# Kernel optimization log

Hardware: AMD Instinct MI355X
Metric: run time of the kernel (lower is better)

Reference implementation:

```python
import jax, jax.numpy as jnp
import numpy as np
from jax import lax


def setup_inputs() -> dict:
    key = jax.random.key(0)
    ks = jax.random.split(key, 13)
    B, L, H, E, V, T = 32, 256, 512, 512, 32000, 64
    s = 0.05
    return {
        "z": jax.random.normal(ks[0], (B, L), jnp.float32),
        "embedding": jax.random.normal(ks[1], (V, E), jnp.float32) * s,
        "Wh": jax.random.normal(ks[2], (H, L), jnp.float32) * s,
        "bh": jax.random.normal(ks[3], (H,), jnp.float32) * s,
        "Wc": jax.random.normal(ks[4], (H, L), jnp.float32) * s,
        "bc": jax.random.normal(ks[5], (H,), jnp.float32) * s,
        "Wih": jax.random.normal(ks[6], (4 * H, E), jnp.float32) * s,
        "Whh": jax.random.normal(ks[7], (4 * H, H), jnp.float32) * s,
        "bih": jax.random.normal(ks[8], (4 * H,), jnp.float32) * s,
        "bhh": jax.random.normal(ks[9], (4 * H,), jnp.float32) * s,
        "Wfc": jax.random.normal(ks[10], (V, H), jnp.float32) * s,
        "bfc": jax.random.normal(ks[11], (V,), jnp.float32) * s,
        "context_length": T,
    }


def reference(z, embedding, Wh, bh, Wc, bc, Wih, Whh, bih, bhh, Wfc, bfc, context_length):
    # project latent to initial LSTM state: [B, H]
    h0 = z @ Wh.T + bh
    c0 = z @ Wc.T + bc
    b_gates = bih + bhh

    def step(carry, _):
        h, c, x = carry  # each [B, H] / [B, E]
        gates = x @ Wih.T + h @ Whh.T + b_gates  # [B, 4H] (pytorch gate order i,f,g,o)
        i, f, g, o = jnp.split(gates, 4, axis=-1)
        c_new = jax.nn.sigmoid(f) * c + jax.nn.sigmoid(i) * jnp.tanh(g)
        h_new = jax.nn.sigmoid(o) * jnp.tanh(c_new)
        logits = h_new @ Wfc.T + bfc  # [B, V]
        pred = jnp.argmax(logits, axis=-1)  # greedy token
        x_new = embedding[pred]  # [B, E]
        return (h_new, c_new, x_new), logits

    # first step feeds h itself as the input (x is None in torch code)
    _, logits = lax.scan(step, (h0, c0, h0), None, length=context_length)
    return jnp.transpose(logits, (1, 0, 2))  # [B, T, V]
```

## Files before the change

### kernel.cpp

```cpp
#include <hip/hip_runtime.h>
#include <hip/hip_bf16.h>
#include <cstdint>
#include <cstddef>

#define NB 32
#define NL 256
#define NH 512
#define NE 512
#define NV 32000
#define NT 64
#define NJ 2048
#define NK 1024
#define NKT 16

typedef __attribute__((ext_vector_type(8))) short bf16x8;
typedef __attribute__((ext_vector_type(4))) float f32x4;


__device__ __forceinline__ unsigned int sortable_f32(float f) {
  unsigned int s = __float_as_uint(f);
  return (s & 0x80000000u) ? ~s : (s | 0x80000000u);
}

__device__ __forceinline__ unsigned long long pack_key(float f, int v) {
  return ((unsigned long long)sortable_f32(f) << 32) |
         (unsigned long long)(unsigned int)(~v);
}

__device__ __forceinline__ unsigned long long shfl_xor_u64(unsigned long long x, int m) {
  unsigned int lo = (unsigned int)x;
  unsigned int hi = (unsigned int)(x >> 32);
  lo = __shfl_xor(lo, m, 64);
  hi = __shfl_xor(hi, m, 64);
  return ((unsigned long long)hi << 32) | lo;
}

__device__ __forceinline__ uint32_t pack_hi16(uint32_t u0, uint32_t u1) {
  return __builtin_amdgcn_perm(u1, u0, 0x07060302u);
}

__device__ __forceinline__ void split3(float4 wa, float4 wb,
                                       bf16x8& A1, bf16x8& A2, bf16x8& A3) {
  union U { uint32_t w[4]; bf16x8 v; };
  U u1, u2, u3;
  float e[8] = {wa.x, wa.y, wa.z, wa.w, wb.x, wb.y, wb.z, wb.w};
#pragma unroll
  for (int p = 0; p < 4; ++p) {
    float e0 = e[2 * p], e1 = e[2 * p + 1];
    uint32_t a0 = __float_as_uint(e0), a1 = __float_as_uint(e1);
    u1.w[p] = pack_hi16(a0, a1);
    float r0 = e0 - __uint_as_float(a0 & 0xffff0000u);
    float r1 = e1 - __uint_as_float(a1 & 0xffff0000u);
    uint32_t b0 = __float_as_uint(r0), b1 = __float_as_uint(r1);
    u2.w[p] = pack_hi16(b0, b1);
    float q0 = r0 - __uint_as_float(b0 & 0xffff0000u);
    float q1 = r1 - __uint_as_float(b1 & 0xffff0000u);
    u3.w[p] = pack_hi16(__float_as_uint(q0), __float_as_uint(q1));
  }
  A1 = u1.v; A2 = u2.v; A3 = u3.v;
}

__device__ __forceinline__ unsigned long long load_key(const unsigned long long* p) {
  return __hip_atomic_load(p, __ATOMIC_ACQUIRE, __HIP_MEMORY_SCOPE_AGENT);
}


__global__ void k_init(const float* __restrict__ z, const float* __restrict__ Wh,
                       const float* __restrict__ bh, const float* __restrict__ Wc,
                       const float* __restrict__ bc, float* __restrict__ hbuf,
                       float* __restrict__ cbuf, unsigned long long* __restrict__ keys) {
  int idx = blockIdx.x * 256 + threadIdx.x;
  int b = idx >> 9, hh = idx & 511;
  const float* zr  = z + b * NL;
  const float* whr = Wh + hh * NL;
  const float* wcr = Wc + hh * NL;
  float ah = 0.f, ac = 0.f;
  for (int k = 0; k < NL; ++k) {
    float zv = zr[k];
    ah += zv * whr[k];
    ac += zv * wcr[k];
  }
  hbuf[b * NH + hh] = ah + bh[hh];
  cbuf[b * NH + hh] = ac + bc[hh];
  if (idx < 64)
    __hip_atomic_store(&keys[idx], 0ULL, __ATOMIC_RELEASE, __HIP_MEMORY_SCOPE_AGENT);
}

__global__ void k_transposeW(const float* __restrict__ Wih, const float* __restrict__ Whh,
                             float* __restrict__ WT) {
  __shared__ float tile[32][33];
  int j0 = blockIdx.x * 32;
  int k0 = blockIdx.y * 32;
  int tx = threadIdx.x & 31;
  int ty = threadIdx.x >> 5;
  for (int r = ty; r < 32; r += 8) {
    int j = j0 + r, k = k0 + tx;
    tile[r][tx] = (k < NE) ? Wih[j * NE + k] : Whh[j * NH + (k - NE)];
  }
  __syncthreads();
  for (int r = ty; r < 32; r += 8) {
    int k = k0 + r, j = j0 + tx;
    WT[(size_t)k * NJ + j] = tile[tx][r];
  }
}

__global__ void k_packW32(const float* __restrict__ Wfc, float* __restrict__ Wp32) {
  int bid = blockIdx.x;
  int tid = threadIdx.x;
  int lane = tid & 63, wv = tid >> 6;
  int r16 = lane & 15, g = lane >> 4;
  const float* wr = Wfc + (size_t)(bid * 16 + r16) * NH + g * 8;
#pragma unroll
  for (int q = 0; q < 4; ++q) {
    int kq = wv * 4 + q;
    float4 wa = *(const float4*)(wr + kq * 32);
    float4 wb = *(const float4*)(wr + kq * 32 + 4);
    float* dst = Wp32 + ((size_t)(bid * 16 + kq) << 9) + lane * 8;
    *(float4*)dst = wa;
    *(float4*)(dst + 4) = wb;
  }
}

__global__ void k_gates(const float* __restrict__ WT, const float* __restrict__ emb,
                        const float* __restrict__ hbuf, const unsigned long long* __restrict__ keys,
                        float* __restrict__ partials, int step) {
  __shared__ unsigned int spred[NB];
  int tid  = threadIdx.x;
  int jthr = tid & 31, bthr = tid >> 5;
  int j0 = blockIdx.x * 128 + jthr * 4;
  int k0 = blockIdx.y * 64;
  int b0 = bthr * 4;
  const float* hin = hbuf + (size_t)(step & 1) * NB * NH;
  const bool isx = (k0 < NE);

  if (step > 0 && isx && tid < NB) {
    unsigned long long key = load_key(&keys[((step - 1) & 1) * NB + tid]);
    unsigned int pred = ~(unsigned int)(key & 0xFFFFFFFFu);
    if (pred >= NV) pred = 0;
    spred[tid] = pred;
  }
  __syncthreads();

  const float* xp[4];
#pragma unroll
  for (int i = 0; i < 4; ++i) {
    int b = b0 + i;
    if (!isx) {
      xp[i] = hin + (size_t)b * NH - NE;
    } else if (step == 0) {
      xp[i] = hin + (size_t)b * NE;
    } else {
      xp[i] = emb + (size_t)spred[b] * NE;
    }
  }

  float acc[4][4];
#pragma unroll
  for (int jj = 0; jj < 4; ++jj)
#pragma unroll
    for (int i = 0; i < 4; ++i) acc[jj][i] = 0.f;

#pragma unroll 4
  for (int k = k0; k < k0 + 64; ++k) {
    float4 w = *(const float4*)(WT + (size_t)k * NJ + j0);
#pragma unroll
    for (int i = 0; i < 4; ++i) {
      float xv = xp[i][k];
      acc[0][i] += w.x * xv;
      acc[1][i] += w.y * xv;
      acc[2][i] += w.z * xv;
      acc[3][i] += w.w * xv;
    }
  }

  int kt = blockIdx.y;
#pragma unroll
  for (int jj = 0; jj < 4; ++jj)
#pragma unroll
    for (int i = 0; i < 4; ++i)
      partials[((size_t)(j0 + jj) * NB + (b0 + i)) * NKT + kt] = acc[jj][i];
}

__global__ void k_cell(const float* __restrict__ partials, const float* __restrict__ bih,
                       const float* __restrict__ bhh, float* __restrict__ hbuf,
                       float* __restrict__ cbuf, unsigned short* __restrict__ hs,
                       unsigned long long* __restrict__ keys, int step) {
  int idx = blockIdx.x * 256 + threadIdx.x;
  int b = idx >> 9, hh = idx & 511;
  float g4[4];
#pragma unroll
  for (int g = 0; g < 4; ++g) {
    int j = g * NH + hh;
    const float4* p4 = (const float4*)(partials + ((size_t)j * NB + b) * NKT);
    float4 a0 = p4[0], a1 = p4[1], a2 = p4[2], a3 = p4[3];
    float s = ((a0.x + a0.y) + (a0.z + a0.w)) + ((a1.x + a1.y) + (a1.z + a1.w)) +
              ((a2.x + a2.y) + (a2.z + a2.w)) + ((a3.x + a3.y) + (a3.z + a3.w));
    g4[g] = s + bih[j] + bhh[j];
  }
  float ig = 1.0f / (1.0f + expf(-g4[0]));
  float fg = 1.0f / (1.0f + expf(-g4[1]));
  float gg = tanhf(g4[2]);
  float og = 1.0f / (1.0f + expf(-g4[3]));
  float c  = cbuf[b * NH + hh];
  float cn = fg * c + ig * gg;
  float hn = og * tanhf(cn);
  cbuf[b * NH + hh] = cn;
  hbuf[(size_t)((step + 1) & 1) * NB * NH + b * NH + hh] = hn;

  uint32_t u = __float_as_uint(hn);
  float r1 = hn - __uint_as_float(u & 0xffff0000u);
  uint32_t u2 = __float_as_uint(r1);
  float r2 = r1 - __uint_as_float(u2 & 0xffff0000u);
  uint32_t u3 = __float_as_uint(r2);
  hs[0 * NB * NH + b * NH + hh] = (unsigned short)(u >> 16);
  hs[1 * NB * NH + b * NH + hh] = (unsigned short)(u2 >> 16);
  hs[2 * NB * NH + b * NH + hh] = (unsigned short)(u3 >> 16);

  if (idx < NB)
    __hip_atomic_store(&keys[(step & 1) * NB + idx], 0ULL,
                       __ATOMIC_RELEASE, __HIP_MEMORY_SCOPE_AGENT);
}

__global__ __launch_bounds__(512, 1) void k_logits3(
    const float* __restrict__ Wp32, const float* __restrict__ bfc,
    const unsigned short* __restrict__ hs, float* __restrict__ out,
    unsigned long long* __restrict__ keys, int step) {
  __shared__ __align__(16) unsigned short H[3][32][520];
  __shared__ __align__(16) float tbuf[32][132];
  __shared__ unsigned long long kmax[32];

  const int tid = threadIdx.x, bid = blockIdx.x;
  const int lane = tid & 63, wid = tid >> 6;
  const int r16 = lane & 15, g = lane >> 4;

  const int wg = bid * 8 + wid;
  const float* wbase = Wp32 + ((size_t)wg << 13) + lane * 8;

  float4 wa0 = *(const float4*)(wbase);
  float4 wb0 = *(const float4*)(wbase + 4);
  float4 wan = *(const float4*)(wbase + 512);
  float4 wbn = *(const float4*)(wbase + 512 + 4);

#pragma unroll
  for (int i = 0; i < 12; ++i) {
    int idx = tid + i * 512;
    int s = idx >> 11, rem = idx & 2047;
    int row = rem >> 6, ch = rem & 63;
    float4 d = *(const float4*)(hs + (size_t)s * (NB * NH) + row * NH + ch * 8);
    *(float4*)(&H[s][row][ch * 8]) = d;
  }
  if (tid < 32) kmax[tid] = 0ULL;

  bf16x8 Acur[3];
  split3(wa0, wb0, Acur[0], Acur[1], Acur[2]);
  __syncthreads();

  f32x4 acc0 = {0.f, 0.f, 0.f, 0.f};
  f32x4 acc1 = {0.f, 0.f, 0.f, 0.f};

#pragma unroll
  for (int kq = 0; kq < 16; ++kq) {
    float4 wa2, wb2;
    if (kq < 14) {
      wa2 = *(const float4*)(wbase + (size_t)(kq + 2) * 512);
      wb2 = *(const float4*)(wbase + (size_t)(kq + 2) * 512 + 4);
    }
    bf16x8 Anx[3];
    if (kq < 15) split3(wan, wbn, Anx[0], Anx[1], Anx[2]);

    const int ko = kq * 32 + g * 8;
    bf16x8 B1n0 = *(const bf16x8*)(&H[0][r16][ko]);
    bf16x8 B1n1 = *(const bf16x8*)(&H[0][r16 + 16][ko]);
    bf16x8 B2n0 = *(const bf16x8*)(&H[1][r16][ko]);
    bf16x8 B2n1 = *(const bf16x8*)(&H[1][r16 + 16][ko]);
    bf16x8 B3n0 = *(const bf16x8*)(&H[2][r16][ko]);
    bf16x8 B3n1 = *(const bf16x8*)(&H[2][r16 + 16][ko]);

    acc0 = __builtin_amdgcn_mfma_f32_16x16x32_bf16(Acur[0], B1n0, acc0, 0, 0, 0);
    acc0 = __builtin_amdgcn_mfma_f32_16x16x32_bf16(Acur[0], B2n0, acc0, 0, 0, 0);
    acc0 = __builtin_amdgcn_mfma_f32_16x16x32_bf16(Acur[1], B1n0, acc0, 0, 0, 0);
    acc0 = __builtin_amdgcn_mfma_f32_16x16x32_bf16(Acur[1], B2n0, acc0, 0, 0, 0);
    acc0 = __builtin_amdgcn_mfma_f32_16x16x32_bf16(Acur[0], B3n0, acc0, 0, 0, 0);
    acc0 = __builtin_amdgcn_mfma_f32_16x16x32_bf16(Acur[2], B1n0, acc0, 0, 0, 0);

    acc1 = __builtin_amdgcn_mfma_f32_16x16x32_bf16(Acur[0], B1n1, acc1, 0, 0, 0);
    acc1 = __builtin_amdgcn_mfma_f32_16x16x32_bf16(Acur[0], B2n1, acc1, 0, 0, 0);
    acc1 = __builtin_amdgcn_mfma_f32_16x16x32_bf16(Acur[1], B1n1, acc1, 0, 0, 0);
    acc1 = __builtin_amdgcn_mfma_f32_16x16x32_bf16(Acur[1], B2n1, acc1, 0, 0, 0);
    acc1 = __builtin_amdgcn_mfma_f32_16x16x32_bf16(Acur[0], B3n1, acc1, 0, 0, 0);
    acc1 = __builtin_amdgcn_mfma_f32_16x16x32_bf16(Acur[2], B1n1, acc1, 0, 0, 0);

    if (kq < 15) {
#pragma unroll
      for (int s = 0; s < 3; ++s) Acur[s] = Anx[s];
      wan = wa2; wbn = wb2;
    }
  }

  const int vwave = bid * 128 + wid * 16;
  float4 bv = *(const float4*)(bfc + vwave + g * 4);
  float lg0[4], lg1[4];
  unsigned long long key0 = 0ULL, key1 = 0ULL;
#pragma unroll
  for (int reg = 0; reg < 4; ++reg) {
    int v = vwave + 4 * g + reg;
    float bvr = (reg == 0) ? bv.x : (reg == 1) ? bv.y : (reg == 2) ? bv.z : bv.w;
    lg0[reg] = acc0[reg] + bvr;
    lg1[reg] = acc1[reg] + bvr;
    unsigned long long p0 = pack_key(lg0[reg], v);
    unsigned long long p1 = pack_key(lg1[reg], v);
    key0 = (p0 > key0) ? p0 : key0;
    key1 = (p1 > key1) ? p1 : key1;
  }
#pragma unroll
  for (int m = 16; m <= 32; m <<= 1) {
    unsigned long long o0 = shfl_xor_u64(key0, m);
    unsigned long long o1 = shfl_xor_u64(key1, m);
    key0 = (o0 > key0) ? o0 : key0;
    key1 = (o1 > key1) ? o1 : key1;
  }
  if (g == 0) {
    atomicMax(&kmax[r16], key0);
    atomicMax(&kmax[r16 + 16], key1);
  }
  __syncthreads();

#pragma unroll
  for (int reg = 0; reg < 4; ++reg) {
    int vloc = wid * 16 + 4 * g + reg;
    tbuf[r16][vloc] = lg0[reg];
    tbuf[r16 + 16][vloc] = lg1[reg];
  }
  __syncthreads();

  {
    int bb = tid >> 4, seg = tid & 15;
    f32x4 p0 = *(const f32x4*)(&tbuf[bb][seg * 8]);
    f32x4 p1 = *(const f32x4*)(&tbuf[bb][seg * 8 + 4]);
    float* dst = out + ((size_t)bb * NT + step) * NV + bid * 128 + seg * 8;
    __builtin_nontemporal_store(p0, (f32x4*)dst);
    __builtin_nontemporal_store(p1, (f32x4*)(dst + 4));
  }
  if (tid < 32) atomicMax(&keys[(step & 1) * NB + tid], kmax[tid]);
}


extern "C" void kernel_launch(void* const* d_in, const int* in_sizes, int n_in,
                              void* d_out, int out_size, void* d_ws, size_t ws_size,
                              hipStream_t stream) {
  (void)in_sizes; (void)n_in; (void)out_size; (void)ws_size;
  const float* z   = (const float*)d_in[0];
  const float* emb = (const float*)d_in[1];
  const float* Wh  = (const float*)d_in[2];
  const float* bh  = (const float*)d_in[3];
  const float* Wc  = (const float*)d_in[4];
  const float* bc  = (const float*)d_in[5];
  const float* Wih = (const float*)d_in[6];
  const float* Whh = (const float*)d_in[7];
  const float* bih = (const float*)d_in[8];
  const float* bhh = (const float*)d_in[9];
  const float* Wfc = (const float*)d_in[10];
  const float* bfc = (const float*)d_in[11];
  float* out = (float*)d_out;

  float* ws = (float*)d_ws;
  float* WT       = ws;
  float* partials = ws + 2097152;
  float* hbuf     = ws + 3145728;
  float* cbuf     = ws + 3178496;
  unsigned long long* keys = (unsigned long long*)(ws + 3194880);
  unsigned short* hs = (unsigned short*)(ws + 3195008);
  float* Wp32 = ws + 3219584;

  k_init<<<64, 256, 0, stream>>>(z, Wh, bh, Wc, bc, hbuf, cbuf, keys);
  k_transposeW<<<dim3(64, 32), 256, 0, stream>>>(Wih, Whh, WT);
  k_packW32<<<2000, 256, 0, stream>>>(Wfc, Wp32);

  for (int t = 0; t < NT; ++t) {
    k_gates<<<dim3(16, 16), 256, 0, stream>>>(WT, emb, hbuf, keys, partials, t);
    k_cell<<<64, 256, 0, stream>>>(partials, bih, bhh, hbuf, cbuf, hs, keys, t);
    k_logits3<<<250, 512, 0, stream>>>(Wp32, bfc, hs, out, keys, t);
  }
}
```

Baseline: 2.747 ms.

## Fuse gate GEMV and LSTM cell kernels with an atomic-counter grid barrier

Merges the gate partial-product kernel and the LSTM cell kernel into one launch of 320 blocks. The first 256 blocks compute partials and bump a global counter, and the last 64 blocks spin until the counter reaches the step's target before doing the cell update. This removes one kernel launch and its boundary per timestep. In exchange it relies on all 320 blocks being co-resident to avoid deadlock, and it adds spin-wait overhead.

```diff
diff --git a/kernel.cpp b/kernel.cpp
--- a/kernel.cpp
+++ b/kernel.cpp
@@ -68,7 +68,8 @@
 __global__ void k_init(const float* __restrict__ z, const float* __restrict__ Wh,
                        const float* __restrict__ bh, const float* __restrict__ Wc,
                        const float* __restrict__ bc, float* __restrict__ hbuf,
-                       float* __restrict__ cbuf, unsigned long long* __restrict__ keys) {
+                       float* __restrict__ cbuf, unsigned long long* __restrict__ keys,
+                       unsigned int* __restrict__ counter) {
   int idx = blockIdx.x * 256 + threadIdx.x;
   int b = idx >> 9, hh = idx & 511;
   const float* zr  = z + b * NL;
@@ -84,6 +85,8 @@
   cbuf[b * NH + hh] = ac + bc[hh];
   if (idx < 64)
     __hip_atomic_store(&keys[idx], 0ULL, __ATOMIC_RELEASE, __HIP_MEMORY_SCOPE_AGENT);
+  if (idx == 64)
+    __hip_atomic_store(counter, 0u, __ATOMIC_RELEASE, __HIP_MEMORY_SCOPE_AGENT);
 }
 
 __global__ void k_transposeW(const float* __restrict__ Wih, const float* __restrict__ Whh,
@@ -121,104 +124,120 @@
   }
 }
 
-__global__ void k_gates(const float* __restrict__ WT, const float* __restrict__ emb,
-                        const float* __restrict__ hbuf, const unsigned long long* __restrict__ keys,
-                        float* __restrict__ partials, int step) {
+__global__ __launch_bounds__(256) void k_gc(
+    const float* __restrict__ WT, const float* __restrict__ emb,
+    const float* __restrict__ hbuf, unsigned long long* __restrict__ keys,
+    float* __restrict__ partials, const float* __restrict__ bih,
+    const float* __restrict__ bhh, float* __restrict__ hbuf_w,
+    float* __restrict__ cbuf, unsigned short* __restrict__ hs,
+    unsigned int* __restrict__ counter, int step) {
   __shared__ unsigned int spred[NB];
-  int tid  = threadIdx.x;
-  int jthr = tid & 31, bthr = tid >> 5;
-  int j0 = blockIdx.x * 128 + jthr * 4;
-  int k0 = blockIdx.y * 64;
-  int b0 = bthr * 4;
-  const float* hin = hbuf + (size_t)(step & 1) * NB * NH;
-  const bool isx = (k0 < NE);
-
-  if (step > 0 && isx && tid < NB) {
-    unsigned long long key = load_key(&keys[((step - 1) & 1) * NB + tid]);
-    unsigned int pred = ~(unsigned int)(key & 0xFFFFFFFFu);
-    if (pred >= NV) pred = 0;
-    spred[tid] = pred;
-  }
-  __syncthreads();
-
-  const float* xp[4];
-#pragma unroll
-  for (int i = 0; i < 4; ++i) {
-    int b = b0 + i;
-    if (!isx) {
-      xp[i] = hin + (size_t)b * NH - NE;
-    } else if (step == 0) {
-      xp[i] = hin + (size_t)b * NE;
-    } else {
-      xp[i] = emb + (size_t)spred[b] * NE;
-    }
-  }
-
-  float acc[4][4];
-#pragma unroll
-  for (int jj = 0; jj < 4; ++jj)
-#pragma unroll
-    for (int i = 0; i < 4; ++i) acc[jj][i] = 0.f;
+  const int tid = threadIdx.x;
+  const int bid = blockIdx.x;
+
+  if (bid < 256) {
+    const int jx = bid & 15, ktb = bid >> 4;
+    int jthr = tid & 31, bthr = tid >> 5;
+    int j0 = jx * 128 + jthr * 4;
+    int k0 = ktb * 64;
+    int b0 = bthr * 4;
+    const float* hin = hbuf + (size_t)(step & 1) * NB * NH;
+    const bool isx = (k0 < NE);
+
+    if (step > 0 && isx && tid < NB) {
+      unsigned long long key = load_key(&keys[((step - 1) & 1) * NB + tid]);
+      unsigned int pred = ~(unsigned int)(key & 0xFFFFFFFFu);
+      if (pred >= NV) pred = 0;
+      spred[tid] = pred;
+    }
+    __syncthreads();
+
+    const float* xp[4];
+#pragma unroll
+    for (int i = 0; i < 4; ++i) {
+      int b = b0 + i;
+      if (!isx) {
+        xp[i] = hin + (size_t)b * NH - NE;
+      } else if (step == 0) {
+        xp[i] = hin + (size_t)b * NE;
+      } else {
+        xp[i] = emb + (size_t)spred[b] * NE;
+      }
+    }
+
+    float acc[4][4];
+#pragma unroll
+    for (int jj = 0; jj < 4; ++jj)
+#pragma unroll
+      for (int i = 0; i < 4; ++i) acc[jj][i] = 0.f;
 
 #pragma unroll 4
-  for (int k = k0; k < k0 + 64; ++k) {
-    float4 w = *(const float4*)(WT + (size_t)k * NJ + j0);
-#pragma unroll
-    for (int i = 0; i < 4; ++i) {
-      float xv = xp[i][k];
-      acc[0][i] += w.x * xv;
-      acc[1][i] += w.y * xv;
-      acc[2][i] += w.z * xv;
-      acc[3][i] += w.w * xv;
-    }
-  }
-
-  int kt = blockIdx.y;
-#pragma unroll
-  for (int jj = 0; jj < 4; ++jj)
-#pragma unroll
-    for (int i = 0; i < 4; ++i)
-      partials[((size_t)(j0 + jj) * NB + (b0 + i)) * NKT + kt] = acc[jj][i];
-}
-
-__global__ void k_cell(const float* __restrict__ partials, const float* __restrict__ bih,
-                       const float* __restrict__ bhh, float* __restrict__ hbuf,
-                       float* __restrict__ cbuf, unsigned short* __restrict__ hs,
-                       unsigned long long* __restrict__ keys, int step) {
-  int idx = blockIdx.x * 256 + threadIdx.x;
-  int b = idx >> 9, hh = idx & 511;
-  float g4[4];
-#pragma unroll
-  for (int g = 0; g < 4; ++g) {
-    int j = g * NH + hh;
-    const float4* p4 = (const float4*)(partials + ((size_t)j * NB + b) * NKT);
-    float4 a0 = p4[0], a1 = p4[1], a2 = p4[2], a3 = p4[3];
-    float s = ((a0.x + a0.y) + (a0.z + a0.w)) + ((a1.x + a1.y) + (a1.z + a1.w)) +
-              ((a2.x + a2.y) + (a2.z + a2.w)) + ((a3.x + a3.y) + (a3.z + a3.w));
-    g4[g] = s + bih[j] + bhh[j];
-  }
-  float ig = 1.0f / (1.0f + expf(-g4[0]));
-  float fg = 1.0f / (1.0f + expf(-g4[1]));
-  float gg = tanhf(g4[2]);
-  float og = 1.0f / (1.0f + expf(-g4[3]));
-  float c  = cbuf[b * NH + hh];
-  float cn = fg * c + ig * gg;
-  float hn = og * tanhf(cn);
-  cbuf[b * NH + hh] = cn;
-  hbuf[(size_t)((step + 1) & 1) * NB * NH + b * NH + hh] = hn;
-
-  uint32_t u = __float_as_uint(hn);
-  float r1 = hn - __uint_as_float(u & 0xffff0000u);
-  uint32_t u2 = __float_as_uint(r1);
-  float r2 = r1 - __uint_as_float(u2 & 0xffff0000u);
-  uint32_t u3 = __float_as_uint(r2);
-  hs[0 * NB * NH + b * NH + hh] = (unsigned short)(u >> 16);
-  hs[1 * NB * NH + b * NH + hh] = (unsigned short)(u2 >> 16);
-  hs[2 * NB * NH + b * NH + hh] = (unsigned short)(u3 >> 16);
-
-  if (idx < NB)
-    __hip_atomic_store(&keys[(step & 1) * NB + idx], 0ULL,
-                       __ATOMIC_RELEASE, __HIP_MEMORY_SCOPE_AGENT);
+    for (int k = k0; k < k0 + 64; ++k) {
+      float4 w = *(const float4*)(WT + (size_t)k * NJ + j0);
+#pragma unroll
+      for (int i = 0; i < 4; ++i) {
+        float xv = xp[i][k];
+        acc[0][i] += w.x * xv;
+        acc[1][i] += w.y * xv;
+        acc[2][i] += w.z * xv;
+        acc[3][i] += w.w * xv;
+      }
+    }
+
+#pragma unroll
+    for (int jj = 0; jj < 4; ++jj)
+#pragma unroll
+      for (int i = 0; i < 4; ++i)
+        partials[((size_t)(j0 + jj) * NB + (b0 + i)) * NKT + ktb] = acc[jj][i];
+
+    __threadfence();
+    __syncthreads();
+    if (tid == 0) atomicAdd(counter, 1u);
+  } else {
+    const unsigned int target = 256u * (unsigned int)(step + 1);
+    if (tid == 0) {
+      while (__hip_atomic_load(counter, __ATOMIC_ACQUIRE, __HIP_MEMORY_SCOPE_AGENT) < target)
+        __builtin_amdgcn_s_sleep(8);
+    }
+    __syncthreads();
+    (void)__hip_atomic_load(counter, __ATOMIC_ACQUIRE, __HIP_MEMORY_SCOPE_AGENT);
+
+    const int cb = bid - 256;
+    int idx = cb * 256 + tid;
+    int b = idx >> 9, hh = idx & 511;
+    float g4[4];
+#pragma unroll
+    for (int g = 0; g < 4; ++g) {
+      int j = g * NH + hh;
+      const float4* p4 = (const float4*)(partials + ((size_t)j * NB + b) * NKT);
+      float4 a0 = p4[0], a1 = p4[1], a2 = p4[2], a3 = p4[3];
+      float s = ((a0.x + a0.y) + (a0.z + a0.w)) + ((a1.x + a1.y) + (a1.z + a1.w)) +
+                ((a2.x + a2.y) + (a2.z + a2.w)) + ((a3.x + a3.y) + (a3.z + a3.w));
+      g4[g] = s + bih[j] + bhh[j];
+    }
+    float ig = 1.0f / (1.0f + expf(-g4[0]));
+    float fg = 1.0f / (1.0f + expf(-g4[1]));
+    float gg = tanhf(g4[2]);
+    float og = 1.0f / (1.0f + expf(-g4[3]));
+    float c  = cbuf[b * NH + hh];
+    float cn = fg * c + ig * gg;
+    float hn = og * tanhf(cn);
+    cbuf[b * NH + hh] = cn;
+    hbuf_w[(size_t)((step + 1) & 1) * NB * NH + b * NH + hh] = hn;
+
+    uint32_t u = __float_as_uint(hn);
+    float r1 = hn - __uint_as_float(u & 0xffff0000u);
+    uint32_t u2 = __float_as_uint(r1);
+    float r2 = r1 - __uint_as_float(u2 & 0xffff0000u);
+    uint32_t u3 = __float_as_uint(r2);
+    hs[0 * NB * NH + b * NH + hh] = (unsigned short)(u >> 16);
+    hs[1 * NB * NH + b * NH + hh] = (unsigned short)(u2 >> 16);
+    hs[2 * NB * NH + b * NH + hh] = (unsigned short)(u3 >> 16);
+
+    if (idx < NB)
+      __hip_atomic_store(&keys[(step & 1) * NB + idx], 0ULL,
+                         __ATOMIC_RELEASE, __HIP_MEMORY_SCOPE_AGENT);
+  }
 }
 
 __global__ __launch_bounds__(512, 1) void k_logits3(
@@ -371,14 +390,15 @@
   unsigned long long* keys = (unsigned long long*)(ws + 3194880);
   unsigned short* hs = (unsigned short*)(ws + 3195008);
   float* Wp32 = ws + 3219584;
-
-  k_init<<<64, 256, 0, stream>>>(z, Wh, bh, Wc, bc, hbuf, cbuf, keys);
+  unsigned int* counter = (unsigned int*)(ws + 19603584);
+
+  k_init<<<64, 256, 0, stream>>>(z, Wh, bh, Wc, bc, hbuf, cbuf, keys, counter);
   k_transposeW<<<dim3(64, 32), 256, 0, stream>>>(Wih, Whh, WT);
   k_packW32<<<2000, 256, 0, stream>>>(Wfc, Wp32);
 
   for (int t = 0; t < NT; ++t) {
-    k_gates<<<dim3(16, 16), 256, 0, stream>>>(WT, emb, hbuf, keys, partials, t);
-    k_cell<<<64, 256, 0, stream>>>(partials, bih, bhh, hbuf, cbuf, hs, keys, t);
+    k_gc<<<320, 256, 0, stream>>>(WT, emb, hbuf, keys, partials, bih, bhh,
+                                  hbuf, cbuf, hs, counter, t);
     k_logits3<<<250, 512, 0, stream>>>(Wp32, bfc, hs, out, keys, t);
   }
 }
```

Result: slower. 5.776 ms (+110.3%).
